# Optimization experiments

Hardware: AMD Instinct MI355X
Metric: run time of the kernel (lower is better)

## Reference

```python
import jax, jax.numpy as jnp
import numpy as np


def setup_inputs() -> dict:
    key = jax.random.key(0)
    k1, k2, k3, k4 = jax.random.split(key, 4)
    B, S, DIN, DOUT = 4, 2048, 4096, 4096
    x = jax.random.normal(k1, (B, S, DIN), dtype=jnp.float32)
    # base is already transposed in the module: [in_features, out_features]
    base = jax.random.normal(k2, (DIN, DOUT), dtype=jnp.float32) * 0.02
    # logical 0/1 bit mask (unpacked view of the packed binary mask), [in, out]
    mask = jax.random.randint(k3, (DIN, DOUT), 0, 2, dtype=jnp.int32)
    # learned scalar coefficient (mean |diff| quantile at init)
    coeff = jax.random.uniform(k4, (), dtype=jnp.float32) * 0.01
    return {"x": x, "base": base, "mask": mask, "coeff": coeff}


def reference(x, base, mask, coeff):
    # binary_bmm: bit 1 -> +1, bit 0 -> -1 sign matrix, shared across batch
    sign = (2 * mask - 1).astype(x.dtype)          # [in, out]
    dense = jnp.einsum("bsi,io->bso", x, base)     # standard dense matmul
    binary = jnp.einsum("bsi,io->bso", x, sign)    # 1-bit (sign) matmul
    return dense + coeff * binary
```

## Files before the change

kernel.cpp:

```cpp
#include <hip/hip_runtime.h>
#include <hip/hip_bf16.h>
#include <stdint.h>


typedef short bf16x8_t __attribute__((ext_vector_type(8)));
typedef float f32x4_t __attribute__((ext_vector_type(4)));
typedef unsigned short u16x8_t __attribute__((ext_vector_type(8)));

#define GLD_LDS16(gptr, lptr)                                                        \
  __builtin_amdgcn_global_load_lds(                                                  \
      (const __attribute__((address_space(1))) void*)(gptr),                         \
      (__attribute__((address_space(3))) void*)(lptr), 16, 0, 0)

#define MFMA_BF16 __builtin_amdgcn_mfma_f32_16x16x32_bf16

__global__ __launch_bounds__(256) void cast_x_kernel(const float* __restrict__ x,
                                                     __hip_bfloat16* __restrict__ xb) {
  size_t i = ((size_t)blockIdx.x * 256 + threadIdx.x) * 8;
  f32x4_t v0 = *(const f32x4_t*)&x[i];
  f32x4_t v1 = *(const f32x4_t*)&x[i + 4];
  __hip_bfloat16 tmp[8];
#pragma unroll
  for (int j = 0; j < 4; ++j) tmp[j] = __float2bfloat16(v0[j]);
#pragma unroll
  for (int j = 0; j < 4; ++j) tmp[4 + j] = __float2bfloat16(v1[j]);
  *(u16x8_t*)&xb[i] = *(const u16x8_t*)tmp;
}

__global__ __launch_bounds__(256) void make_wt_kernel(const float* __restrict__ base,
                                                      const int* __restrict__ mask,
                                                      const float* __restrict__ coeffp,
                                                      __hip_bfloat16* __restrict__ wt,
                                                      int K, int N) {
  __shared__ float tile[32][33];
  const float coeff = coeffp[0];
  const int n0 = blockIdx.x * 32, k0 = blockIdx.y * 32;
  const int tx = threadIdx.x & 31;
  const int ty = threadIdx.x >> 5;
#pragma unroll
  for (int j = 0; j < 4; ++j) {
    int k = k0 + ty + j * 8;
    size_t idx = (size_t)k * N + n0 + tx;
    float b = base[idx];
    int m = mask[idx];
    tile[ty + j * 8][tx] = b + (m ? coeff : -coeff);
  }
  __syncthreads();
#pragma unroll
  for (int j = 0; j < 4; ++j) {
    int n = n0 + ty + j * 8;
    wt[(size_t)n * K + k0 + tx] = __float2bfloat16(tile[tx][ty + j * 8]);
  }
}

__global__ __launch_bounds__(512, 2) void gemm256_kernel(const __hip_bfloat16* __restrict__ xb,
                                                         const __hip_bfloat16* __restrict__ wt,
                                                         float* __restrict__ out,
                                                         int M, int N, int K) {
  __shared__ __align__(16) __hip_bfloat16 As[2 * 256 * 64];
  __shared__ __align__(16) __hip_bfloat16 Bs[2 * 256 * 64];
  const int NT = K >> 6;

  const int nwg = gridDim.x;
  int bid = blockIdx.x;
  int sw = bid;
  if ((nwg & 7) == 0) {
    int per = nwg >> 3;
    sw = (bid & 7) * per + (bid >> 3);
  }
  const int ntn = N >> 8;
  const int tm = sw / ntn, tn = sw - tm * ntn;
  const int m0 = tm << 8, n0 = tn << 8;

  const int tid = threadIdx.x;
  const int lane = tid & 63;
  const int wave = tid >> 6;
  const int wr = wave >> 2;
  const int wc = wave & 3;

  const int lrow = lane >> 3;
  const int lcol = ((lane & 7) ^ lrow) << 3;
  uint32_t aOff[2][2], bOff[2][2];
#pragma unroll
  for (int h = 0; h < 2; ++h)
#pragma unroll
    for (int j = 0; j < 2; ++j) {
      aOff[h][j] = (uint32_t)((m0 + h * 128 + wave * 16 + j * 8 + lrow) * K + lcol);
      bOff[h][j] = (uint32_t)((n0 + h * 128 + wave * 16 + j * 8 + lrow) * K + lcol);
    }

#define STAGE_A(h, j, tau)                                                       \
  GLD_LDS16(xb + (size_t)aOff[h][j] + (size_t)(tau) * 64,                        \
            (char*)As + (((tau) & 1) << 15) + ((h) * 16384 + wave * 2048 + (j) * 1024))
#define STAGE_B(h, j, tau)                                                       \
  GLD_LDS16(wt + (size_t)bOff[h][j] + (size_t)(tau) * 64,                        \
            (char*)Bs + (((tau) & 1) << 15) + ((h) * 16384 + wave * 2048 + (j) * 1024))

  STAGE_A(0, 0, 0); STAGE_A(0, 1, 0);
  STAGE_A(1, 0, 0); STAGE_A(1, 1, 0);
  STAGE_B(0, 0, 0); STAGE_B(0, 1, 0);
  STAGE_B(1, 0, 0); STAGE_B(1, 1, 0);
  STAGE_A(0, 0, 1); STAGE_A(0, 1, 1);
  asm volatile("s_waitcnt vmcnt(2)" ::: "memory");
  __builtin_amdgcn_s_barrier();

  const int lane15 = lane & 15;
  const int swz = (lane & 7) << 4;
  const int c0 = (((lane >> 4) << 4)) ^ swz;
  const int c1 = (64 + ((lane >> 4) << 4)) ^ swz;
  const int aRowB = (wr * 128 + lane15) * 128;
  const int bRowB = (wc * 64 + lane15) * 128;

  f32x4_t acc[8][4];
  const f32x4_t zero = {0.0f, 0.0f, 0.0f, 0.0f};
#pragma unroll
  for (int i = 0; i < 8; ++i)
#pragma unroll
    for (int j = 0; j < 4; ++j) acc[i][j] = zero;

  bf16x8_t aL[4][2], aH[4][2], bL[2][2], bH[2][2];

  for (int t = 0; t < NT; ++t) {
    const int p = t & 1;
    const char* a0 = (const char*)As + (p << 15) + aRowB;
    const char* b0 = (const char*)Bs + (p << 15) + bRowB;

#pragma unroll
    for (int mi = 0; mi < 4; ++mi) {
      aL[mi][0] = *(const bf16x8_t*)(a0 + mi * 2048 + c0);
      aL[mi][1] = *(const bf16x8_t*)(a0 + mi * 2048 + c1);
    }
#pragma unroll
    for (int ni = 0; ni < 2; ++ni) {
      bL[ni][0] = *(const bf16x8_t*)(b0 + ni * 2048 + c0);
      bL[ni][1] = *(const bf16x8_t*)(b0 + ni * 2048 + c1);
      bH[ni][0] = *(const bf16x8_t*)(b0 + (ni + 2) * 2048 + c0);
      bH[ni][1] = *(const bf16x8_t*)(b0 + (ni + 2) * 2048 + c1);
    }
    if (t + 1 < NT) {
      STAGE_A(1, 0, t + 1); STAGE_A(1, 1, t + 1);
      STAGE_B(0, 0, t + 1); STAGE_B(0, 1, t + 1);
      STAGE_B(1, 0, t + 1); STAGE_B(1, 1, t + 1);
    }
    asm volatile("s_waitcnt lgkmcnt(0)" ::: "memory");
    __builtin_amdgcn_sched_barrier(0);
    __builtin_amdgcn_s_setprio(1);
#pragma unroll
    for (int mi = 0; mi < 4; ++mi)
#pragma unroll
      for (int ni = 0; ni < 2; ++ni) {
        acc[mi][ni] = MFMA_BF16(aL[mi][0], bL[ni][0], acc[mi][ni], 0, 0, 0);
        acc[mi][ni] = MFMA_BF16(aL[mi][1], bL[ni][1], acc[mi][ni], 0, 0, 0);
        acc[mi][ni + 2] = MFMA_BF16(aL[mi][0], bH[ni][0], acc[mi][ni + 2], 0, 0, 0);
        acc[mi][ni + 2] = MFMA_BF16(aL[mi][1], bH[ni][1], acc[mi][ni + 2], 0, 0, 0);
      }
    __builtin_amdgcn_s_setprio(0);
    __builtin_amdgcn_s_barrier();

#pragma unroll
    for (int mi = 0; mi < 4; ++mi) {
      aH[mi][0] = *(const bf16x8_t*)(a0 + (mi + 4) * 2048 + c0);
      aH[mi][1] = *(const bf16x8_t*)(a0 + (mi + 4) * 2048 + c1);
    }
    if (t + 2 < NT) { STAGE_A(0, 0, t + 2); STAGE_A(0, 1, t + 2); }
    asm volatile("s_waitcnt lgkmcnt(0)" ::: "memory");
    __builtin_amdgcn_sched_barrier(0);
    __builtin_amdgcn_s_setprio(1);
#pragma unroll
    for (int mi = 0; mi < 4; ++mi)
#pragma unroll
      for (int ni = 0; ni < 2; ++ni) {
        acc[mi + 4][ni + 2] = MFMA_BF16(aH[mi][0], bH[ni][0], acc[mi + 4][ni + 2], 0, 0, 0);
        acc[mi + 4][ni + 2] = MFMA_BF16(aH[mi][1], bH[ni][1], acc[mi + 4][ni + 2], 0, 0, 0);
        acc[mi + 4][ni] = MFMA_BF16(aH[mi][0], bL[ni][0], acc[mi + 4][ni], 0, 0, 0);
        acc[mi + 4][ni] = MFMA_BF16(aH[mi][1], bL[ni][1], acc[mi + 4][ni], 0, 0, 0);
      }
    __builtin_amdgcn_s_setprio(0);
    if (t + 2 < NT)      asm volatile("s_waitcnt vmcnt(2)" ::: "memory");
    else if (t + 1 < NT) asm volatile("s_waitcnt vmcnt(0)" ::: "memory");
    __builtin_amdgcn_s_barrier();
  }

  const int row0 = m0 + wr * 128 + (lane >> 4) * 4;
  const int col0 = n0 + wc * 64 + lane15;
#pragma unroll
  for (int mi = 0; mi < 8; ++mi)
#pragma unroll
    for (int ni = 0; ni < 4; ++ni) {
#pragma unroll
      for (int k = 0; k < 4; ++k)
        out[(size_t)(row0 + mi * 16 + k) * N + col0 + ni * 16] = acc[mi][ni][k];
    }
#undef STAGE_A
#undef STAGE_B
}

__global__ __launch_bounds__(256) void gemm_fallback_kernel(const float* __restrict__ x,
                                                            const float* __restrict__ base,
                                                            const int* __restrict__ mask,
                                                            const float* __restrict__ coeffp,
                                                            float* __restrict__ out,
                                                            int M, int N, int K) {
  __shared__ __align__(16) __hip_bfloat16 As[128 * 32];
  __shared__ __align__(16) __hip_bfloat16 Bs[128 * 32];
  const float coeff = coeffp[0];
  const int ntn = N >> 7;
  const int tm = blockIdx.x / ntn, tn = blockIdx.x - tm * ntn;
  const int m0 = tm << 7, n0 = tn << 7;
  const int tid = threadIdx.x, lane = tid & 63, wave = tid >> 6;
  const int wr = wave >> 1, wc = wave & 1;

  f32x4_t acc[4][4];
  const f32x4_t zero = {0.0f, 0.0f, 0.0f, 0.0f};
#pragma unroll
  for (int i = 0; i < 4; ++i)
#pragma unroll
    for (int j = 0; j < 4; ++j) acc[i][j] = zero;

  const int arow = tid >> 1;
  const int acol = (tid & 1) * 16;
  const int bkk = tid & 31;
  const int bnb = (tid >> 5) * 16;
  const int arow_base = wr * 64 + (lane & 15);
  const int bcol_base = wc * 64 + (lane & 15);
  const int koff = (lane >> 4) * 8;

  for (int k0 = 0; k0 < K; k0 += 32) {
    __syncthreads();
    {
      const float* src = &x[(size_t)(m0 + arow) * K + k0 + acol];
      __hip_bfloat16 tmp[16];
#pragma unroll
      for (int j = 0; j < 16; ++j) tmp[j] = __float2bfloat16(src[j]);
      *(u16x8_t*)&As[arow * 32 + acol] = *(const u16x8_t*)&tmp[0];
      *(u16x8_t*)&As[arow * 32 + acol + 8] = *(const u16x8_t*)&tmp[8];
    }
    {
      const float* bsrc = &base[(size_t)(k0 + bkk) * N + n0 + bnb];
      const int* msrc = &mask[(size_t)(k0 + bkk) * N + n0 + bnb];
#pragma unroll
      for (int j = 0; j < 16; ++j) {
        float w = bsrc[j] + (msrc[j] ? coeff : -coeff);
        Bs[(bnb + j) * 32 + bkk] = __float2bfloat16(w);
      }
    }
    __syncthreads();

    bf16x8_t a[4], b[4];
#pragma unroll
    for (int mi = 0; mi < 4; ++mi)
      a[mi] = *(const bf16x8_t*)&As[(arow_base + mi * 16) * 32 + koff];
#pragma unroll
    for (int ni = 0; ni < 4; ++ni)
      b[ni] = *(const bf16x8_t*)&Bs[(bcol_base + ni * 16) * 32 + koff];
#pragma unroll
    for (int mi = 0; mi < 4; ++mi)
#pragma unroll
      for (int ni = 0; ni < 4; ++ni)
        acc[mi][ni] = MFMA_BF16(a[mi], b[ni], acc[mi][ni], 0, 0, 0);
  }

  const int row0 = m0 + wr * 64 + (lane >> 4) * 4;
  const int col0 = n0 + wc * 64 + (lane & 15);
#pragma unroll
  for (int mi = 0; mi < 4; ++mi)
#pragma unroll
    for (int ni = 0; ni < 4; ++ni) {
      int r = row0 + mi * 16;
      int c = col0 + ni * 16;
#pragma unroll
      for (int k = 0; k < 4; ++k) out[(size_t)(r + k) * N + c] = acc[mi][ni][k];
    }
}

extern "C" void kernel_launch(void* const* d_in, const int* in_sizes, int n_in,
                              void* d_out, int out_size, void* d_ws, size_t ws_size,
                              hipStream_t stream) {
  const int B = 4, S = 2048, DIN = 4096, DOUT = 4096;
  const int M = B * S;
  const float* x = (const float*)d_in[0];
  const float* base = (const float*)d_in[1];
  const int* mask = (const int*)d_in[2];
  const float* coeff = (const float*)d_in[3];
  float* out = (float*)d_out;

  const size_t xb_bytes = (size_t)M * DIN * sizeof(__hip_bfloat16);
  const size_t wt_bytes = (size_t)DIN * DOUT * sizeof(__hip_bfloat16);

  if (ws_size >= xb_bytes + wt_bytes) {
    __hip_bfloat16* xb = (__hip_bfloat16*)d_ws;
    __hip_bfloat16* wt = (__hip_bfloat16*)((char*)d_ws + xb_bytes);
    cast_x_kernel<<<(M * DIN) / (256 * 8), 256, 0, stream>>>(x, xb);
    make_wt_kernel<<<dim3(DOUT / 32, DIN / 32), 256, 0, stream>>>(base, mask, coeff, wt, DIN, DOUT);
    const int n_tiles = (M / 256) * (DOUT / 256);
    gemm256_kernel<<<n_tiles, 512, 0, stream>>>(xb, wt, out, M, DOUT, DIN);
  } else {
    const int n_tiles = (M / 128) * (DOUT / 128);
    gemm_fallback_kernel<<<n_tiles, 256, 0, stream>>>(x, base, mask, coeff, out, M, DOUT, DIN);
  }
}
```

Before: 304.9 us.

## Simplify GEMM pipeline to whole-tile double buffering with one barrier per step

```diff
diff --git a/kernel.cpp b/kernel.cpp
--- a/kernel.cpp
+++ b/kernel.cpp
@@ -96,12 +96,16 @@
   GLD_LDS16(wt + (size_t)bOff[h][j] + (size_t)(tau) * 64,                        \
             (char*)Bs + (((tau) & 1) << 15) + ((h) * 16384 + wave * 2048 + (j) * 1024))
 
-  STAGE_A(0, 0, 0); STAGE_A(0, 1, 0);
-  STAGE_A(1, 0, 0); STAGE_A(1, 1, 0);
-  STAGE_B(0, 0, 0); STAGE_B(0, 1, 0);
-  STAGE_B(1, 0, 0); STAGE_B(1, 1, 0);
-  STAGE_A(0, 0, 1); STAGE_A(0, 1, 1);
-  asm volatile("s_waitcnt vmcnt(2)" ::: "memory");
+#define STAGE_TILE(tau)                                                          \
+  do {                                                                           \
+    STAGE_A(0, 0, tau); STAGE_A(0, 1, tau);                                      \
+    STAGE_A(1, 0, tau); STAGE_A(1, 1, tau);                                      \
+    STAGE_B(0, 0, tau); STAGE_B(0, 1, tau);                                      \
+    STAGE_B(1, 0, tau); STAGE_B(1, 1, tau);                                      \
+  } while (0)
+
+  STAGE_TILE(0);
+  asm volatile("s_waitcnt vmcnt(0)" ::: "memory");
   __builtin_amdgcn_s_barrier();
 
   const int lane15 = lane & 15;
@@ -125,10 +129,14 @@
     const char* a0 = (const char*)As + (p << 15) + aRowB;
     const char* b0 = (const char*)Bs + (p << 15) + bRowB;
 
+    if (t + 1 < NT) STAGE_TILE(t + 1);
+
 #pragma unroll
     for (int mi = 0; mi < 4; ++mi) {
       aL[mi][0] = *(const bf16x8_t*)(a0 + mi * 2048 + c0);
       aL[mi][1] = *(const bf16x8_t*)(a0 + mi * 2048 + c1);
+      aH[mi][0] = *(const bf16x8_t*)(a0 + (mi + 4) * 2048 + c0);
+      aH[mi][1] = *(const bf16x8_t*)(a0 + (mi + 4) * 2048 + c1);
     }
 #pragma unroll
     for (int ni = 0; ni < 2; ++ni) {
@@ -137,11 +145,6 @@
       bH[ni][0] = *(const bf16x8_t*)(b0 + (ni + 2) * 2048 + c0);
       bH[ni][1] = *(const bf16x8_t*)(b0 + (ni + 2) * 2048 + c1);
     }
-    if (t + 1 < NT) {
-      STAGE_A(1, 0, t + 1); STAGE_A(1, 1, t + 1);
-      STAGE_B(0, 0, t + 1); STAGE_B(0, 1, t + 1);
-      STAGE_B(1, 0, t + 1); STAGE_B(1, 1, t + 1);
-    }
     asm volatile("s_waitcnt lgkmcnt(0)" ::: "memory");
     __builtin_amdgcn_sched_barrier(0);
     __builtin_amdgcn_s_setprio(1);
@@ -153,31 +156,13 @@
         acc[mi][ni] = MFMA_BF16(aL[mi][1], bL[ni][1], acc[mi][ni], 0, 0, 0);
         acc[mi][ni + 2] = MFMA_BF16(aL[mi][0], bH[ni][0], acc[mi][ni + 2], 0, 0, 0);
         acc[mi][ni + 2] = MFMA_BF16(aL[mi][1], bH[ni][1], acc[mi][ni + 2], 0, 0, 0);
-      }
-    __builtin_amdgcn_s_setprio(0);
-    __builtin_amdgcn_s_barrier();
-
-#pragma unroll
-    for (int mi = 0; mi < 4; ++mi) {
-      aH[mi][0] = *(const bf16x8_t*)(a0 + (mi + 4) * 2048 + c0);
-      aH[mi][1] = *(const bf16x8_t*)(a0 + (mi + 4) * 2048 + c1);
-    }
-    if (t + 2 < NT) { STAGE_A(0, 0, t + 2); STAGE_A(0, 1, t + 2); }
-    asm volatile("s_waitcnt lgkmcnt(0)" ::: "memory");
-    __builtin_amdgcn_sched_barrier(0);
-    __builtin_amdgcn_s_setprio(1);
-#pragma unroll
-    for (int mi = 0; mi < 4; ++mi)
-#pragma unroll
-      for (int ni = 0; ni < 2; ++ni) {
         acc[mi + 4][ni + 2] = MFMA_BF16(aH[mi][0], bH[ni][0], acc[mi + 4][ni + 2], 0, 0, 0);
         acc[mi + 4][ni + 2] = MFMA_BF16(aH[mi][1], bH[ni][1], acc[mi + 4][ni + 2], 0, 0, 0);
         acc[mi + 4][ni] = MFMA_BF16(aH[mi][0], bL[ni][0], acc[mi + 4][ni], 0, 0, 0);
         acc[mi + 4][ni] = MFMA_BF16(aH[mi][1], bL[ni][1], acc[mi + 4][ni], 0, 0, 0);
       }
     __builtin_amdgcn_s_setprio(0);
-    if (t + 2 < NT)      asm volatile("s_waitcnt vmcnt(2)" ::: "memory");
-    else if (t + 1 < NT) asm volatile("s_waitcnt vmcnt(0)" ::: "memory");
+    if (t + 1 < NT) asm volatile("s_waitcnt vmcnt(0)" ::: "memory");
     __builtin_amdgcn_s_barrier();
   }
 
@@ -191,6 +176,7 @@
       for (int k = 0; k < 4; ++k)
         out[(size_t)(row0 + mi * 16 + k) * N + col0 + ni * 16] = acc[mi][ni][k];
     }
+#undef STAGE_TILE
 #undef STAGE_A
 #undef STAGE_B
 }
```

After: 362.6 us. +18.9%, slower.
